# Kernel optimization log

Measured on AMD Instinct MI355X. Metric: run time of the kernel, lower is better.

Reference implementation:

```python
import jax, jax.numpy as jnp
import numpy as np

HIDDEN = 512
EMBED = 512
VOCAB = 32000
BRANCH = 4
LEVELS = 9  # level 0 = root, level LEVELS-1 = leaves (complete 4-ary tree)
N_NODES = sum(BRANCH ** l for l in range(LEVELS))  # 87381


def setup_inputs() -> dict:
    key = jax.random.key(0)
    ks = jax.random.split(key, 16)
    s = 1.0 / np.sqrt(HIDDEN)
    inp = {
        "token_ids": jax.random.randint(ks[0], (N_NODES,), 0, VOCAB, dtype=jnp.int32),
        "emb": jax.random.normal(ks[1], (VOCAB, EMBED), jnp.float32) * 0.02,
        "Wi": jax.random.normal(ks[2], (EMBED, HIDDEN), jnp.float32) * s,
        "Ui": jax.random.normal(ks[3], (HIDDEN, HIDDEN), jnp.float32) * s,
        "bi": jnp.zeros((HIDDEN,), jnp.float32),
        "Wf": jax.random.normal(ks[4], (EMBED, HIDDEN), jnp.float32) * s,
        "Uf": jax.random.normal(ks[5], (HIDDEN, HIDDEN), jnp.float32) * s,
        "bf": jnp.zeros((HIDDEN,), jnp.float32),
        "Wo": jax.random.normal(ks[6], (EMBED, HIDDEN), jnp.float32) * s,
        "Uo": jax.random.normal(ks[7], (HIDDEN, HIDDEN), jnp.float32) * s,
        "bo": jnp.zeros((HIDDEN,), jnp.float32),
        "Wu": jax.random.normal(ks[8], (EMBED, HIDDEN), jnp.float32) * s,
        "Uu": jax.random.normal(ks[9], (HIDDEN, HIDDEN), jnp.float32) * s,
        "bu": jnp.zeros((HIDDEN,), jnp.float32),
        "branching": BRANCH,
        "n_levels": LEVELS,
    }
    return inp


def reference(token_ids, emb, Wi, Ui, bi, Wf, Uf, bf, Wo, Uo, bo, Wu, Uu, bu,
              branching, n_levels):
    # Level-synchronous Child-Sum Tree-LSTM over a complete `branching`-ary tree.
    # token_ids is laid out level by level, root first.
    B = int(branching)
    L = int(n_levels)
    H = Wi.shape[1]
    level_sizes = [B ** l for l in range(L)]
    offsets = np.concatenate([[0], np.cumsum(level_sizes)])  # static Python ints

    # Leaves: original code sets h = c = 0 (leaf embedding is computed but unused).
    h = jnp.zeros((level_sizes[-1], H), dtype=emb.dtype)
    c = jnp.zeros((level_sizes[-1], H), dtype=emb.dtype)
    hs_levels = [h]  # hidden states collected leaves -> root (level order)

    for l in range(L - 2, -1, -1):
        n = level_sizes[l]
        x = jnp.take(emb, token_ids[offsets[l]:offsets[l + 1]], axis=0)  # [n, E]
        ch_h = h.reshape(n, B, H)  # children of node k are contiguous
        ch_c = c.reshape(n, B, H)
        h_tilde = ch_h.sum(axis=1)  # [n, H] child-sum
        i = jax.nn.sigmoid(x @ Wi + h_tilde @ Ui + bi)
        # per-child forget gates: [n, B, H]
        f = jax.nn.sigmoid((x @ Wf + bf)[:, None, :] + ch_h @ Uf)
        o = jax.nn.sigmoid(x @ Wo + h_tilde @ Uo + bo)
        u = jnp.tanh(x @ Wu + h_tilde @ Uu + bu)
        c = i * u + (f * ch_c).sum(axis=1)
        h = o * jnp.tanh(c)
        hs_levels.append(h)

    hidden_states = jnp.concatenate(hs_levels, axis=0)  # [N_NODES, H]
    return hidden_states, h, c  # h, c are the root states, shape [1, H]
```

## Files before the change

### kernel.cpp

```cpp
#include <hip/hip_runtime.h>

#define DI __device__ __forceinline__

typedef __attribute__((ext_vector_type(8))) __bf16 bf16x8;
typedef __attribute__((ext_vector_type(4))) float f32x4;
typedef __attribute__((ext_vector_type(8))) unsigned short ushort8;
typedef unsigned long long ull;

static DI unsigned short f2b(float f) {
  unsigned int x = __builtin_bit_cast(unsigned int, f);
  unsigned int r = (x + 0x7FFFu + ((x >> 16) & 1u)) >> 16;
  return (unsigned short)r;
}
static DI float b2f(unsigned short u) {
  return __builtin_bit_cast(float, (unsigned int)u << 16);
}
static DI float sigmf(float x) { return 1.0f / (1.0f + __expf(-x)); }

typedef const __attribute__((address_space(1))) void* gcptr;
typedef __attribute__((address_space(3))) void* lptr;
static DI void gl_lds16(const void* g, void* l) {
  __builtin_amdgcn_global_load_lds((gcptr)g, (lptr)l, 16, 0, 0);
}

#define GCOL(g, d) ((((d) >> 5) << 7) + ((g) << 5) + ((d) & 31))

static DI size_t qaddr(int NT, int row4, int c) {
  int tm = row4 >> 5, tn = c >> 7;
  int rq = row4 & 31, c7 = c & 127;
  int wv = ((rq >> 4) << 1) | (c7 >> 6);
  int mf = (rq >> 2) & 3, nf = (c7 >> 4) & 3;
  int lane = ((rq & 3) << 4) | (c7 & 15);
  return ((size_t)(tm * NT + tn) << 12) + (size_t)((((wv << 4) + (mf << 2) + nf) << 6) + lane);
}

__global__ void prep_pack(const float* __restrict__ Wi, const float* __restrict__ Ui,
                          const float* __restrict__ bi, const float* __restrict__ Wf,
                          const float* __restrict__ Uf, const float* __restrict__ bfv,
                          const float* __restrict__ Wo, const float* __restrict__ Uo,
                          const float* __restrict__ bo, const float* __restrict__ Wu,
                          const float* __restrict__ Uu, const float* __restrict__ bu,
                          unsigned short* __restrict__ Wp, unsigned short* __restrict__ Upiou,
                          unsigned short* __restrict__ Upf, float* __restrict__ bias)
{
  int u = blockIdx.x * blockDim.x + threadIdx.x;
  if (u < 131072) {
    int k8 = u >> 11, n = u & 2047;
    int gate = (n >> 5) & 3;
    int d = ((n >> 7) << 5) | (n & 31);
    const float* W = (gate == 0) ? Wi : (gate == 1) ? Wf : (gate == 2) ? Wo : Wu;
    ushort8 pk;
    #pragma unroll
    for (int t = 0; t < 8; ++t) pk[t] = f2b(W[(size_t)(k8*8+t)*512 + d]);
    *(ushort8*)&Wp[(size_t)u*8] = pk;
  } else if (u < 131072 + 98304) {
    int v = u - 131072;
    int k8 = v / 1536, n = v - k8*1536;
    const float* U = (n < 512) ? Ui : (n < 1024) ? Uo : Uu;
    int c = n & 511;
    ushort8 pk;
    #pragma unroll
    for (int t = 0; t < 8; ++t) pk[t] = f2b(U[(size_t)(k8*8+t)*512 + c]);
    *(ushort8*)&Upiou[(size_t)v*8] = pk;
  } else {
    int v = u - 229376;
    int k8 = v >> 9, c = v & 511;
    ushort8 pk;
    #pragma unroll
    for (int t = 0; t < 8; ++t) pk[t] = f2b(Uf[(size_t)(k8*8+t)*512 + c]);
    *(ushort8*)&Upf[(size_t)v*8] = pk;
  }
  if (u < 2048) {
    int gate = (u >> 5) & 3;
    int d = ((u >> 7) << 5) | (u & 31);
    bias[u] = (gate == 0) ? bi[d] : (gate == 1) ? bfv[d] : (gate == 2) ? bo[d] : bu[d];
  }
}

__global__ void gather_x(const int* __restrict__ tok, const float* __restrict__ emb,
                         unsigned short* __restrict__ X)
{
  int u = blockIdx.x * blockDim.x + threadIdx.x;
  if (u >= 22272*64) return;
  int R = u >> 6, ch = u & 63;
  int l, node;
  if (R < 512)       { l = R >> 7; node = R & 127; int sz = 1 << (2*l); if (node >= sz) node = sz - 1; }
  else if (R < 768)  { l = 4; node = R - 512; }
  else if (R < 1792) { l = 5; node = R - 768; }
  else if (R < 5888) { l = 6; node = R - 1792; }
  else               { l = 7; node = R - 5888; }
  static const int offs_c[8] = {0,1,5,21,85,341,1365,5461};
  int tk = tok[offs_c[l] + node];
  const float* src = emb + (size_t)tk*512 + ch*8;
  ushort8 pk;
  #pragma unroll
  for (int t = 0; t < 8; ++t) pk[t] = f2b(src[t]);
  *(ushort8*)&X[(size_t)u*8] = pk;
}

struct GDesc {
  const unsigned short* A;
  const unsigned short* Bp;
  ull* C;
  int M, N, NT;
};
struct L7P {
  float* hout; unsigned short* hb; float* cb; unsigned short* ht;
  float* zbase; size_t z4;
};

template<bool FUSED>
__global__ __launch_bounds__(256)
void gemm512(GDesc g1, GDesc g2, int split, const float* __restrict__ bias, L7P l7)
{
  __shared__ float smemf[128*132];
  unsigned short* As = (unsigned short*)smemf;
  unsigned short* Bs = (unsigned short*)smemf + 2*128*64;

  const int nwg = gridDim.x, orig = blockIdx.x;
  const int q = nwg >> 3, r = nwg & 7;
  const int xcd = orig & 7, idx = orig >> 3;
  const int wg = (xcd < r ? xcd*(q+1) : r*(q+1) + (xcd-r)*q) + idx;

  const bool role1 = (wg < split);
  GDesc g = role1 ? g1 : g2;
  const int lwg = role1 ? wg : wg - split;
  const int tm = lwg / g.NT, tn = lwg - tm * g.NT;

  const int tid = threadIdx.x;
  const int wave = tid >> 6, lane = tid & 63;
  const int Mbase = tm * 128, Nbase = tn * 128;
  const int wr = wave >> 1, wc = wave & 1;

  const int arow_l = wave*8 + (lane >> 3);
  const int acol8  = lane & 7;
  const int sw8    = arow_l & 7;

  f32x4 acc[4][4] = {};

  auto STAGE = [&](int p, int k0) {
    #pragma unroll
    for (int c = 0; c < 4; ++c) {
      int grow = Mbase + c*32 + arow_l;
      if (grow >= g.M) grow = g.M - 1;
      gl_lds16(g.A + (size_t)grow*512 + k0 + ((acol8 ^ sw8) * 8),
               As + p*(128*64) + (c*32 + wave*8)*64);
    }
    #pragma unroll
    for (int c = 0; c < 4; ++c) {
      int k8 = c*2 + (wave >> 1);
      int colh = (wave & 1) * 64;
      gl_lds16(g.Bp + ((size_t)((k0 >> 3) + k8) * g.N + Nbase + colh + lane) * 8,
               Bs + p*(8*128*8) + (k8*128 + colh)*8);
    }
  };

  auto COMPUTE = [&](int p) {
    #pragma unroll
    for (int ks = 0; ks < 2; ++ks) {
      bf16x8 af[4], bfr[4];
      #pragma unroll
      for (int mf = 0; mf < 4; ++mf) {
        int row = wr*64 + mf*16 + (lane & 15);
        int kc  = ks*4 + (lane >> 4);
        af[mf] = *(const bf16x8*)&As[p*(128*64) + row*64 + ((kc ^ (row & 7)) * 8)];
      }
      #pragma unroll
      for (int nf = 0; nf < 4; ++nf) {
        int col = wc*64 + nf*16 + (lane & 15);
        int k8  = ks*4 + (lane >> 4);
        bfr[nf] = *(const bf16x8*)&Bs[p*(8*128*8) + (k8*128 + col) * 8];
      }
      #pragma unroll
      for (int mf = 0; mf < 4; ++mf)
        #pragma unroll
        for (int nf = 0; nf < 4; ++nf)
          acc[mf][nf] = __builtin_amdgcn_mfma_f32_16x16x32_bf16(af[mf], bfr[nf], acc[mf][nf], 0, 0, 0);
    }
  };

  STAGE(0, 0);
  __syncthreads();
  #pragma unroll
  for (int it = 0; it < 7; ++it) {
    STAGE((it + 1) & 1, (it + 1) * 64);
    COMPUTE(it & 1);
    __syncthreads();
  }
  COMPUTE(1);

  auto ZERO_DUTY = [&]() {
    if constexpr (FUSED) {
      size_t b4 = (size_t)orig * 3072;
      f32x4 z = {0.f, 0.f, 0.f, 0.f};
      f32x4* zp = (f32x4*)l7.zbase;
      #pragma unroll
      for (int i = 0; i < 12; ++i) {
        size_t off = b4 + (size_t)i*256 + tid;
        if (off < l7.z4) zp[off] = z;
      }
    }
  };

  if (FUSED && tm >= 46) {
    __syncthreads();
    #pragma unroll
    for (int mf = 0; mf < 4; ++mf) {
      int rbase = wr*64 + mf*16 + (lane >> 4)*4;
      #pragma unroll
      for (int nf = 0; nf < 4; ++nf) {
        int col = wc*64 + nf*16 + (lane & 15);
        #pragma unroll
        for (int rr = 0; rr < 4; ++rr)
          smemf[(rbase + rr)*132 + col] = acc[mf][nf][rr];
      }
    }
    __syncthreads();
    ZERO_DUTY();
    const int dlow = tid & 31, rowg = tid >> 5;
    const int d = tn*32 + dlow;
    const float bi_ = bias[tn*128      + dlow];
    const float bo_ = bias[tn*128 + 64 + dlow];
    const float bu_ = bias[tn*128 + 96 + dlow];
    const int nodebase = Mbase - 5888 + rowg*16;
    float hts = 0.f;
    #pragma unroll
    for (int rr = 0; rr < 16; ++rr) {
      int lrow = rowg*16 + rr;
      float gi = smemf[lrow*132      + dlow];
      float go = smemf[lrow*132 + 64 + dlow];
      float gu = smemf[lrow*132 + 96 + dlow];
      float iv = sigmf(gi + bi_), ov = sigmf(go + bo_), uv = tanhf(gu + bu_);
      float cv = iv * uv;
      float hv = ov * tanhf(cv);
      size_t node = nodebase + rr;
      l7.hout[node*512 + d] = hv;
      l7.hb[node*512 + d]   = f2b(hv);
      l7.cb[node*512 + d]   = cv;
      hts += hv;
      if ((rr & 3) == 3) {
        l7.ht[(size_t)((nodebase + rr - 3) >> 2)*512 + d] = f2b(hts);
        hts = 0.f;
      }
    }
  } else {
    ZERO_DUTY();
    float bv[4];
    #pragma unroll
    for (int nf = 0; nf < 4; ++nf)
      bv[nf] = (bias != nullptr && role1) ? bias[Nbase + wc*64 + nf*16 + (lane & 15)] : 0.f;
    ull* Cb = g.C + ((size_t)(tm * g.NT + tn) << 12) + ((size_t)wave << 10);
    #pragma unroll
    for (int mf = 0; mf < 4; ++mf)
      #pragma unroll
      for (int nf = 0; nf < 4; ++nf) {
        f32x4 a = acc[mf][nf];
        ull pk = (ull)f2b(a[0] + bv[nf]) | ((ull)f2b(a[1] + bv[nf]) << 16)
               | ((ull)f2b(a[2] + bv[nf]) << 32) | ((ull)f2b(a[3] + bv[nf]) << 48);
        Cb[(mf*4 + nf)*64 + lane] = pk;
      }
  }
}

__global__ __launch_bounds__(256)
void combine2(const ull* __restrict__ Gq,
              const ull* __restrict__ Rq,
              const ull* __restrict__ Fq,
              const float* __restrict__ cch,
              float* __restrict__ hout,
              unsigned short* __restrict__ hbf,
              float* __restrict__ cout,
              unsigned short* __restrict__ htout,
              float* __restrict__ rootx,
              int n)
{
  const int b = blockIdx.x, t = threadIdx.x;
  #pragma unroll
  for (int half = 0; half < 2; ++half) {
    const int c = t + half * 256;
    ull gi4 = Gq[qaddr(16, b, GCOL(0, c))];
    ull gf4 = Gq[qaddr(16, b, GCOL(1, c))];
    ull go4 = Gq[qaddr(16, b, GCOL(2, c))];
    ull gu4 = Gq[qaddr(16, b, GCOL(3, c))];
    ull ri4 = Rq[qaddr(12, b, c)];
    ull ro4 = Rq[qaddr(12, b, c + 512)];
    ull ru4 = Rq[qaddr(12, b, c + 1024)];
    float hts = 0.f;
    #pragma unroll
    for (int rI = 0; rI < 4; ++rI) {
      int j = b*4 + rI;
      float gi = b2f((unsigned short)(gi4 >> (16*rI)));
      float gf = b2f((unsigned short)(gf4 >> (16*rI)));
      float go = b2f((unsigned short)(go4 >> (16*rI)));
      float gu = b2f((unsigned short)(gu4 >> (16*rI)));
      float iv = sigmf(gi + b2f((unsigned short)(ri4 >> (16*rI))));
      float ov = sigmf(go + b2f((unsigned short)(ro4 >> (16*rI))));
      float uv = tanhf(gu + b2f((unsigned short)(ru4 >> (16*rI))));
      ull f4 = Fq[qaddr(4, j, c)];
      const float* cc = cch + (size_t)(j*4)*512 + c;
      float fs = 0.f;
      #pragma unroll
      for (int k = 0; k < 4; ++k)
        fs += sigmf(gf + b2f((unsigned short)(f4 >> (16*k)))) * cc[(size_t)k*512];
      float cv = iv*uv + fs;
      float hv = ov * tanhf(cv);
      if (j < n) {
        hout[(size_t)j*512 + c] = hv;
        hbf[(size_t)j*512 + c]  = f2b(hv);
        cout[(size_t)j*512 + c] = cv;
        if (rootx && j == 0) { rootx[c] = hv; rootx[512 + c] = cv; }
        hts += hv;
      }
    }
    if (htout) htout[(size_t)b*512 + c] = f2b(hts);
  }
}

extern "C" void kernel_launch(void* const* d_in, const int* in_sizes, int n_in,
                              void* d_out, int out_size, void* d_ws, size_t ws_size,
                              hipStream_t stream)
{
  const int*   tok = (const int*)d_in[0];
  const float* emb = (const float*)d_in[1];
  const float* Wi  = (const float*)d_in[2];
  const float* Ui  = (const float*)d_in[3];
  const float* bi  = (const float*)d_in[4];
  const float* Wf  = (const float*)d_in[5];
  const float* Uf  = (const float*)d_in[6];
  const float* bfv = (const float*)d_in[7];
  const float* Wo  = (const float*)d_in[8];
  const float* Uo  = (const float*)d_in[9];
  const float* bo  = (const float*)d_in[10];
  const float* Wu  = (const float*)d_in[11];
  const float* Uu  = (const float*)d_in[12];
  const float* bu  = (const float*)d_in[13];

  char* ws = (char*)d_ws;
  unsigned short* Wp    = (unsigned short*)(ws + 0);
  unsigned short* Upiou = (unsigned short*)(ws + 2097152);
  unsigned short* Upf   = (unsigned short*)(ws + 3670016);
  float*          bias  = (float*)        (ws + 4194304);
  unsigned short* hbf   = (unsigned short*)(ws + 4202496);
  unsigned short* htbf  = (unsigned short*)(ws + 26571776);
  float*          cbuf  = (float*)        (ws + 32163840);
  ull*            RiouQ = (ull*)          (ws + 76902400);
  ull*            RfQ   = (ull*)          (ws + 89485312);
  ull*            Gq    = (ull*)          (ws + 106262528);
  unsigned short* X     = (unsigned short*)(ws + 130379776);

  float* fout = (float*)d_out;

  static const int  offs[9]    = {0,1,5,21,85,341,1365,5461,21845};
  static const int  padbase[8] = {0,128,256,384,512,768,1792,5888};
  static const long outoff[8]  = {87380,87376,87360,87296,87040,86016,81920,65536};

  prep_pack<<<1024, 256, 0, stream>>>(Wi,Ui,bi,Wf,Uf,bfv,Wo,Uo,bo,Wu,Uu,bu,
                                      Wp,Upiou,Upf,bias);
  gather_x<<<(22272*64)/256, 256, 0, stream>>>(tok, emb, X);

  GDesc gA { X, Wp, Gq, 22272, 2048, 16 };
  L7P l7 { fout + (size_t)outoff[7]*512, hbf + (size_t)offs[7]*512,
           cbuf + (size_t)offs[7]*512, htbf + (size_t)offs[6]*512,
           fout, (size_t)65536*512/4 };
  gemm512<true><<<174*16, 256, 0, stream>>>(gA, gA, 174*16, bias, l7);

  L7P l7n {};
  for (int l = 6; l >= 0; --l) {
    int n = 1 << (2*l);
    int tm1 = (n + 127) / 128, tm2 = (4*n + 127) / 128;
    int split = tm1 * 12;
    GDesc g1 { htbf + (size_t)offs[l]*512,   Upiou, RiouQ, n,   1536, 12 };
    GDesc g2 { hbf  + (size_t)offs[l+1]*512, Upf,   RfQ,   4*n, 512,  4  };
    gemm512<false><<<split + tm2*4, 256, 0, stream>>>(g1, g2, split, nullptr, l7n);
    combine2<<<(n + 3) / 4, 256, 0, stream>>>(
        Gq + (size_t)padbase[l]*512, RiouQ, RfQ, cbuf + (size_t)offs[l+1]*512,
        fout + (size_t)outoff[l]*512, hbf + (size_t)offs[l]*512, cbuf + (size_t)offs[l]*512,
        (l > 0) ? htbf + (size_t)offs[l-1]*512 : nullptr,
        (l == 0) ? fout + (size_t)87381*512 : nullptr,
        n);
  }
}
```

Before: 259.7 us.

## Interleave gates at 16-column granularity and fuse level-7 epilogue in registers

Changes the packed gate column layout from 32-wide to 16-wide groups, so each wave's MFMA output fragment holds all four gates for the same hidden columns. The level-7 epilogue can then compute the LSTM cell directly from accumulators, with no LDS round trip or extra barriers. The GEMM K-step is halved to 32, which shrinks the LDS footprint but doubles the number of pipeline iterations and syncs. Higher occupancy from smaller LDS is traded against more barrier overhead and less strided epilogue stores.

```diff
diff --git a/kernel.cpp b/kernel.cpp
--- a/kernel.cpp
+++ b/kernel.cpp
@@ -23,7 +23,7 @@
   __builtin_amdgcn_global_load_lds((gcptr)g, (lptr)l, 16, 0, 0);
 }
 
-#define GCOL(g, d) ((((d) >> 5) << 7) + ((g) << 5) + ((d) & 31))
+#define GCOL(g, d) ((((d) >> 4) << 6) + ((g) << 4) + ((d) & 15))
 
 static DI size_t qaddr(int NT, int row4, int c) {
   int tm = row4 >> 5, tn = c >> 7;
@@ -46,8 +46,8 @@
   int u = blockIdx.x * blockDim.x + threadIdx.x;
   if (u < 131072) {
     int k8 = u >> 11, n = u & 2047;
-    int gate = (n >> 5) & 3;
-    int d = ((n >> 7) << 5) | (n & 31);
+    int gate = (n >> 4) & 3;
+    int d = ((n >> 6) << 4) | (n & 15);
     const float* W = (gate == 0) ? Wi : (gate == 1) ? Wf : (gate == 2) ? Wo : Wu;
     ushort8 pk;
     #pragma unroll
@@ -71,8 +71,8 @@
     *(ushort8*)&Upf[(size_t)v*8] = pk;
   }
   if (u < 2048) {
-    int gate = (u >> 5) & 3;
-    int d = ((u >> 7) << 5) | (u & 31);
+    int gate = (u >> 4) & 3;
+    int d = ((u >> 6) << 4) | (u & 15);
     bias[u] = (gate == 0) ? bi[d] : (gate == 1) ? bfv[d] : (gate == 2) ? bo[d] : bu[d];
   }
 }
@@ -113,9 +113,8 @@
 __global__ __launch_bounds__(256)
 void gemm512(GDesc g1, GDesc g2, int split, const float* __restrict__ bias, L7P l7)
 {
-  __shared__ float smemf[128*132];
-  unsigned short* As = (unsigned short*)smemf;
-  unsigned short* Bs = (unsigned short*)smemf + 2*128*64;
+  __shared__ unsigned short As[2*128*32];
+  __shared__ unsigned short Bs[2*4*128*8];
 
   const int nwg = gridDim.x, orig = blockIdx.x;
   const int q = nwg >> 3, r = nwg & 7;
@@ -132,58 +131,49 @@
   const int Mbase = tm * 128, Nbase = tn * 128;
   const int wr = wave >> 1, wc = wave & 1;
 
-  const int arow_l = wave*8 + (lane >> 3);
-  const int acol8  = lane & 7;
-  const int sw8    = arow_l & 7;
-
   f32x4 acc[4][4] = {};
 
   auto STAGE = [&](int p, int k0) {
     #pragma unroll
-    for (int c = 0; c < 4; ++c) {
-      int grow = Mbase + c*32 + arow_l;
-      if (grow >= g.M) grow = g.M - 1;
-      gl_lds16(g.A + (size_t)grow*512 + k0 + ((acol8 ^ sw8) * 8),
-               As + p*(128*64) + (c*32 + wave*8)*64);
-    }
-    #pragma unroll
-    for (int c = 0; c < 4; ++c) {
-      int k8 = c*2 + (wave >> 1);
-      int colh = (wave & 1) * 64;
-      gl_lds16(g.Bp + ((size_t)((k0 >> 3) + k8) * g.N + Nbase + colh + lane) * 8,
-               Bs + p*(8*128*8) + (k8*128 + colh)*8);
+    for (int c = 0; c < 2; ++c) {
+      int lrow = c*64 + wave*16 + (lane >> 2);
+      int grow = Mbase + lrow; if (grow >= g.M) grow = g.M - 1;
+      gl_lds16(g.A + (size_t)grow*512 + k0 + (((lane & 3) ^ (lrow & 3)) * 8),
+               As + p*(128*32) + (c*64 + wave*16)*32);
+    }
+    #pragma unroll
+    for (int c = 0; c < 2; ++c) {
+      gl_lds16(g.Bp + ((size_t)((k0 >> 3) + wave) * g.N + Nbase + c*64 + lane) * 8,
+               Bs + p*(4*128*8) + (wave*128 + c*64)*8);
     }
   };
 
   auto COMPUTE = [&](int p) {
-    #pragma unroll
-    for (int ks = 0; ks < 2; ++ks) {
-      bf16x8 af[4], bfr[4];
-      #pragma unroll
-      for (int mf = 0; mf < 4; ++mf) {
-        int row = wr*64 + mf*16 + (lane & 15);
-        int kc  = ks*4 + (lane >> 4);
-        af[mf] = *(const bf16x8*)&As[p*(128*64) + row*64 + ((kc ^ (row & 7)) * 8)];
-      }
-      #pragma unroll
-      for (int nf = 0; nf < 4; ++nf) {
-        int col = wc*64 + nf*16 + (lane & 15);
-        int k8  = ks*4 + (lane >> 4);
-        bfr[nf] = *(const bf16x8*)&Bs[p*(8*128*8) + (k8*128 + col) * 8];
-      }
-      #pragma unroll
-      for (int mf = 0; mf < 4; ++mf)
-        #pragma unroll
-        for (int nf = 0; nf < 4; ++nf)
-          acc[mf][nf] = __builtin_amdgcn_mfma_f32_16x16x32_bf16(af[mf], bfr[nf], acc[mf][nf], 0, 0, 0);
-    }
+    bf16x8 af[4], bfr[4];
+    #pragma unroll
+    for (int mf = 0; mf < 4; ++mf) {
+      int row = wr*64 + mf*16 + (lane & 15);
+      int kc  = lane >> 4;
+      af[mf] = *(const bf16x8*)&As[p*(128*32) + row*32 + ((kc ^ (row & 3)) * 8)];
+    }
+    #pragma unroll
+    for (int nf = 0; nf < 4; ++nf) {
+      int col = wc*64 + nf*16 + (lane & 15);
+      int k8  = lane >> 4;
+      bfr[nf] = *(const bf16x8*)&Bs[p*(4*128*8) + (k8*128 + col) * 8];
+    }
+    #pragma unroll
+    for (int mf = 0; mf < 4; ++mf)
+      #pragma unroll
+      for (int nf = 0; nf < 4; ++nf)
+        acc[mf][nf] = __builtin_amdgcn_mfma_f32_16x16x32_bf16(af[mf], bfr[nf], acc[mf][nf], 0, 0, 0);
   };
 
   STAGE(0, 0);
   __syncthreads();
   #pragma unroll
-  for (int it = 0; it < 7; ++it) {
-    STAGE((it + 1) & 1, (it + 1) * 64);
+  for (int it = 0; it < 15; ++it) {
+    STAGE((it + 1) & 1, (it + 1) * 32);
     COMPUTE(it & 1);
     __syncthreads();
   }
@@ -203,46 +193,31 @@
   };
 
   if (FUSED && tm >= 46) {
-    __syncthreads();
+    const int dlow = lane & 15;
+    const float bi_ = bias[Nbase + wc*64      + dlow];
+    const float bo_ = bias[Nbase + wc*64 + 32 + dlow];
+    const float bu_ = bias[Nbase + wc*64 + 48 + dlow];
+    const int d = tn*32 + wc*16 + dlow;
     #pragma unroll
     for (int mf = 0; mf < 4; ++mf) {
-      int rbase = wr*64 + mf*16 + (lane >> 4)*4;
-      #pragma unroll
-      for (int nf = 0; nf < 4; ++nf) {
-        int col = wc*64 + nf*16 + (lane & 15);
-        #pragma unroll
-        for (int rr = 0; rr < 4; ++rr)
-          smemf[(rbase + rr)*132 + col] = acc[mf][nf][rr];
+      int node0 = Mbase - 5888 + wr*64 + mf*16 + (lane >> 4)*4;
+      float hts = 0.f;
+      #pragma unroll
+      for (int rr = 0; rr < 4; ++rr) {
+        float iv = sigmf(acc[mf][0][rr] + bi_);
+        float ov = sigmf(acc[mf][2][rr] + bo_);
+        float uv = tanhf(acc[mf][3][rr] + bu_);
+        float cv = iv * uv;
+        float hv = ov * tanhf(cv);
+        size_t node = node0 + rr;
+        l7.hout[node*512 + d] = hv;
+        l7.hb[node*512 + d]   = f2b(hv);
+        l7.cb[node*512 + d]   = cv;
+        hts += hv;
       }
-    }
-    __syncthreads();
+      l7.ht[(size_t)(node0 >> 2)*512 + d] = f2b(hts);
+    }
     ZERO_DUTY();
-    const int dlow = tid & 31, rowg = tid >> 5;
-    const int d = tn*32 + dlow;
-    const float bi_ = bias[tn*128      + dlow];
-    const float bo_ = bias[tn*128 + 64 + dlow];
-    const float bu_ = bias[tn*128 + 96 + dlow];
-    const int nodebase = Mbase - 5888 + rowg*16;
-    float hts = 0.f;
-    #pragma unroll
-    for (int rr = 0; rr < 16; ++rr) {
-      int lrow = rowg*16 + rr;
-      float gi = smemf[lrow*132      + dlow];
-      float go = smemf[lrow*132 + 64 + dlow];
-      float gu = smemf[lrow*132 + 96 + dlow];
-      float iv = sigmf(gi + bi_), ov = sigmf(go + bo_), uv = tanhf(gu + bu_);
-      float cv = iv * uv;
-      float hv = ov * tanhf(cv);
-      size_t node = nodebase + rr;
-      l7.hout[node*512 + d] = hv;
-      l7.hb[node*512 + d]   = f2b(hv);
-      l7.cb[node*512 + d]   = cv;
-      hts += hv;
-      if ((rr & 3) == 3) {
-        l7.ht[(size_t)((nodebase + rr - 3) >> 2)*512 + d] = f2b(hts);
-        hts = 0.f;
-      }
-    }
   } else {
     ZERO_DUTY();
     float bv[4];
```

New measurement: 307.1 us. +18.2%, slower.

## Fuse small upper tree levels into one persistent kernel with grid barriers

Applied to the files above, without the earlier changes.

Replaces the per-level GEMM and combine launches for levels 4..0 with a single 64-block persistent kernel. It uses atomic grid barriers and a direct-from-global tile GEMM, which removes many small kernel launches and their gaps. The fused leaf-level epilogue now works on accumulator registers, using a reordered gate interleave instead of an LDS round-trip. Output zeroing moves into the level-6 GEMM. The spin barriers rely on all 64 blocks being co-resident.

```diff
diff --git a/kernel.cpp b/kernel.cpp
--- a/kernel.cpp
+++ b/kernel.cpp
@@ -23,7 +23,7 @@
   __builtin_amdgcn_global_load_lds((gcptr)g, (lptr)l, 16, 0, 0);
 }
 
-#define GCOL(g, d) ((((d) >> 5) << 7) + ((g) << 5) + ((d) & 31))
+#define GCOL(g, d) ((((d) >> 4) << 6) + ((g) << 4) + ((d) & 15))
 
 static DI size_t qaddr(int NT, int row4, int c) {
   int tm = row4 >> 5, tn = c >> 7;
@@ -41,13 +41,15 @@
                           const float* __restrict__ bo, const float* __restrict__ Wu,
                           const float* __restrict__ Uu, const float* __restrict__ bu,
                           unsigned short* __restrict__ Wp, unsigned short* __restrict__ Upiou,
-                          unsigned short* __restrict__ Upf, float* __restrict__ bias)
+                          unsigned short* __restrict__ Upf, float* __restrict__ bias,
+                          unsigned int* __restrict__ bar)
 {
   int u = blockIdx.x * blockDim.x + threadIdx.x;
+  if (u < 16) bar[u] = 0u;
   if (u < 131072) {
     int k8 = u >> 11, n = u & 2047;
-    int gate = (n >> 5) & 3;
-    int d = ((n >> 7) << 5) | (n & 31);
+    int gate = (n >> 4) & 3;
+    int d = ((n >> 6) << 4) | (n & 15);
     const float* W = (gate == 0) ? Wi : (gate == 1) ? Wf : (gate == 2) ? Wo : Wu;
     ushort8 pk;
     #pragma unroll
@@ -71,8 +73,8 @@
     *(ushort8*)&Upf[(size_t)v*8] = pk;
   }
   if (u < 2048) {
-    int gate = (u >> 5) & 3;
-    int d = ((u >> 7) << 5) | (u & 31);
+    int gate = (u >> 4) & 3;
+    int d = ((u >> 6) << 4) | (u & 15);
     bias[u] = (gate == 0) ? bi[d] : (gate == 1) ? bfv[d] : (gate == 2) ? bo[d] : bu[d];
   }
 }
@@ -106,16 +108,15 @@
 };
 struct L7P {
   float* hout; unsigned short* hb; float* cb; unsigned short* ht;
-  float* zbase; size_t z4;
 };
 
 template<bool FUSED>
 __global__ __launch_bounds__(256)
-void gemm512(GDesc g1, GDesc g2, int split, const float* __restrict__ bias, L7P l7)
-{
-  __shared__ float smemf[128*132];
-  unsigned short* As = (unsigned short*)smemf;
-  unsigned short* Bs = (unsigned short*)smemf + 2*128*64;
+void gemm512(GDesc g1, GDesc g2, int split, const float* __restrict__ bias, L7P l7,
+             float* __restrict__ zbase, size_t z4)
+{
+  __shared__ unsigned short As[2*128*64];
+  __shared__ unsigned short Bs[2*8*128*8];
 
   const int nwg = gridDim.x, orig = blockIdx.x;
   const int q = nwg >> 3, r = nwg & 7;
@@ -131,6 +132,7 @@
   const int wave = tid >> 6, lane = tid & 63;
   const int Mbase = tm * 128, Nbase = tn * 128;
   const int wr = wave >> 1, wc = wave & 1;
+  const int l15 = lane & 15, l4 = lane >> 4;
 
   const int arow_l = wave*8 + (lane >> 3);
   const int acol8  = lane & 7;
@@ -161,14 +163,14 @@
       bf16x8 af[4], bfr[4];
       #pragma unroll
       for (int mf = 0; mf < 4; ++mf) {
-        int row = wr*64 + mf*16 + (lane & 15);
-        int kc  = ks*4 + (lane >> 4);
+        int row = wr*64 + mf*16 + l15;
+        int kc  = ks*4 + l4;
         af[mf] = *(const bf16x8*)&As[p*(128*64) + row*64 + ((kc ^ (row & 7)) * 8)];
       }
       #pragma unroll
       for (int nf = 0; nf < 4; ++nf) {
-        int col = wc*64 + nf*16 + (lane & 15);
-        int k8  = ks*4 + (lane >> 4);
+        int col = wc*64 + nf*16 + l15;
+        int k8  = ks*4 + l4;
         bfr[nf] = *(const bf16x8*)&Bs[p*(8*128*8) + (k8*128 + col) * 8];
       }
       #pragma unroll
@@ -189,66 +191,35 @@
   }
   COMPUTE(1);
 
-  auto ZERO_DUTY = [&]() {
-    if constexpr (FUSED) {
-      size_t b4 = (size_t)orig * 3072;
-      f32x4 z = {0.f, 0.f, 0.f, 0.f};
-      f32x4* zp = (f32x4*)l7.zbase;
-      #pragma unroll
-      for (int i = 0; i < 12; ++i) {
-        size_t off = b4 + (size_t)i*256 + tid;
-        if (off < l7.z4) zp[off] = z;
+  if (FUSED && tm >= 46) {
+    const float bi_ = bias[Nbase + wc*64      + l15];
+    const float bo_ = bias[Nbase + wc*64 + 32 + l15];
+    const float bu_ = bias[Nbase + wc*64 + 48 + l15];
+    const int d = tn*32 + wc*16 + l15;
+    #pragma unroll
+    for (int mf = 0; mf < 4; ++mf) {
+      int node0 = Mbase - 5888 + wr*64 + mf*16 + l4*4;
+      float hts = 0.f;
+      #pragma unroll
+      for (int rr = 0; rr < 4; ++rr) {
+        float iv = sigmf(acc[mf][0][rr] + bi_);
+        float ov = sigmf(acc[mf][2][rr] + bo_);
+        float uv = tanhf(acc[mf][3][rr] + bu_);
+        float cv = iv * uv;
+        float hv = ov * tanhf(cv);
+        size_t node = node0 + rr;
+        l7.hout[node*512 + d] = hv;
+        l7.hb[node*512 + d]   = f2b(hv);
+        l7.cb[node*512 + d]   = cv;
+        hts += hv;
       }
-    }
-  };
-
-  if (FUSED && tm >= 46) {
-    __syncthreads();
-    #pragma unroll
-    for (int mf = 0; mf < 4; ++mf) {
-      int rbase = wr*64 + mf*16 + (lane >> 4)*4;
-      #pragma unroll
-      for (int nf = 0; nf < 4; ++nf) {
-        int col = wc*64 + nf*16 + (lane & 15);
-        #pragma unroll
-        for (int rr = 0; rr < 4; ++rr)
-          smemf[(rbase + rr)*132 + col] = acc[mf][nf][rr];
-      }
-    }
-    __syncthreads();
-    ZERO_DUTY();
-    const int dlow = tid & 31, rowg = tid >> 5;
-    const int d = tn*32 + dlow;
-    const float bi_ = bias[tn*128      + dlow];
-    const float bo_ = bias[tn*128 + 64 + dlow];
-    const float bu_ = bias[tn*128 + 96 + dlow];
-    const int nodebase = Mbase - 5888 + rowg*16;
-    float hts = 0.f;
-    #pragma unroll
-    for (int rr = 0; rr < 16; ++rr) {
-      int lrow = rowg*16 + rr;
-      float gi = smemf[lrow*132      + dlow];
-      float go = smemf[lrow*132 + 64 + dlow];
-      float gu = smemf[lrow*132 + 96 + dlow];
-      float iv = sigmf(gi + bi_), ov = sigmf(go + bo_), uv = tanhf(gu + bu_);
-      float cv = iv * uv;
-      float hv = ov * tanhf(cv);
-      size_t node = nodebase + rr;
-      l7.hout[node*512 + d] = hv;
-      l7.hb[node*512 + d]   = f2b(hv);
-      l7.cb[node*512 + d]   = cv;
-      hts += hv;
-      if ((rr & 3) == 3) {
-        l7.ht[(size_t)((nodebase + rr - 3) >> 2)*512 + d] = f2b(hts);
-        hts = 0.f;
-      }
+      l7.ht[(size_t)(node0 >> 2)*512 + d] = f2b(hts);
     }
   } else {
-    ZERO_DUTY();
     float bv[4];
     #pragma unroll
     for (int nf = 0; nf < 4; ++nf)
-      bv[nf] = (bias != nullptr && role1) ? bias[Nbase + wc*64 + nf*16 + (lane & 15)] : 0.f;
+      bv[nf] = (bias != nullptr && role1) ? bias[Nbase + wc*64 + nf*16 + l15] : 0.f;
     ull* Cb = g.C + ((size_t)(tm * g.NT + tn) << 12) + ((size_t)wave << 10);
     #pragma unroll
     for (int mf = 0; mf < 4; ++mf)
@@ -260,21 +231,21 @@
         Cb[(mf*4 + nf)*64 + lane] = pk;
       }
   }
-}
-
-__global__ __launch_bounds__(256)
-void combine2(const ull* __restrict__ Gq,
-              const ull* __restrict__ Rq,
-              const ull* __restrict__ Fq,
-              const float* __restrict__ cch,
-              float* __restrict__ hout,
-              unsigned short* __restrict__ hbf,
-              float* __restrict__ cout,
-              unsigned short* __restrict__ htout,
-              float* __restrict__ rootx,
-              int n)
-{
-  const int b = blockIdx.x, t = threadIdx.x;
+
+  if (zbase != nullptr) {
+    f32x4 z = {0.f, 0.f, 0.f, 0.f};
+    f32x4* zp = (f32x4*)zbase;
+    size_t stride = (size_t)nwg * 256;
+    for (size_t off = (size_t)orig*256 + tid; off < z4; off += stride) zp[off] = z;
+  }
+}
+
+static DI void combine_body(const ull* __restrict__ Gq, const ull* __restrict__ Rq,
+                            const ull* __restrict__ Fq, const float* __restrict__ cch,
+                            float* __restrict__ hout, unsigned short* __restrict__ hbf,
+                            float* __restrict__ cout, unsigned short* __restrict__ htout,
+                            float* __restrict__ rootx, int n, int b, int t)
+{
   #pragma unroll
   for (int half = 0; half < 2; ++half) {
     const int c = t + half * 256;
@@ -313,6 +284,108 @@
       }
     }
     if (htout) htout[(size_t)b*512 + c] = f2b(hts);
+  }
+}
+
+__global__ __launch_bounds__(256)
+void combine2(const ull* Gq, const ull* Rq, const ull* Fq, const float* cch,
+              float* hout, unsigned short* hbf, float* cout,
+              unsigned short* htout, float* rootx, int n)
+{
+  combine_body(Gq, Rq, Fq, cch, hout, hbf, cout, htout, rootx, n, blockIdx.x, threadIdx.x);
+}
+
+static DI void gbar(unsigned int* c, unsigned int target) {
+  __syncthreads();
+  if (threadIdx.x == 0) {
+    __hip_atomic_fetch_add(c, 1u, __ATOMIC_ACQ_REL, __HIP_MEMORY_SCOPE_AGENT);
+    while (__hip_atomic_load(c, __ATOMIC_ACQUIRE, __HIP_MEMORY_SCOPE_AGENT) < target) {}
+  }
+  __syncthreads();
+}
+
+static DI void tile_gemm(const unsigned short* __restrict__ A, int M,
+                         const unsigned short* __restrict__ Bp, int N, int NT,
+                         int tm, int tn, ull* __restrict__ C, int wave, int lane)
+{
+  const int wr = wave >> 1, wc = wave & 1;
+  const int l15 = lane & 15, l4 = lane >> 4;
+  size_t a0[4]; unsigned int b0[4];
+  #pragma unroll
+  for (int mf = 0; mf < 4; ++mf) {
+    int row = tm*128 + wr*64 + mf*16 + l15;
+    if (row >= M) row = M - 1;
+    a0[mf] = (size_t)row*512 + l4*8;
+  }
+  #pragma unroll
+  for (int nf = 0; nf < 4; ++nf)
+    b0[nf] = (unsigned int)(((unsigned)l4 * N + tn*128 + wc*64 + nf*16 + l15) * 8);
+  const unsigned int bstep = (unsigned int)N * 32;
+
+  f32x4 acc[4][4] = {};
+  #pragma unroll
+  for (int ks = 0; ks < 16; ++ks) {
+    bf16x8 af[4], bfr[4];
+    #pragma unroll
+    for (int mf = 0; mf < 4; ++mf) af[mf] = *(const bf16x8*)(A + a0[mf] + ks*32);
+    #pragma unroll
+    for (int nf = 0; nf < 4; ++nf) bfr[nf] = *(const bf16x8*)(Bp + b0[nf] + ks*bstep);
+    #pragma unroll
+    for (int mf = 0; mf < 4; ++mf)
+      #pragma unroll
+      for (int nf = 0; nf < 4; ++nf)
+        acc[mf][nf] = __builtin_amdgcn_mfma_f32_16x16x32_bf16(af[mf], bfr[nf], acc[mf][nf], 0, 0, 0);
+  }
+  ull* Cb = C + ((size_t)(tm * NT + tn) << 12) + ((size_t)wave << 10);
+  #pragma unroll
+  for (int mf = 0; mf < 4; ++mf)
+    #pragma unroll
+    for (int nf = 0; nf < 4; ++nf) {
+      f32x4 a = acc[mf][nf];
+      ull pk = (ull)f2b(a[0]) | ((ull)f2b(a[1]) << 16)
+             | ((ull)f2b(a[2]) << 32) | ((ull)f2b(a[3]) << 48);
+      Cb[(mf*4 + nf)*64 + lane] = pk;
+    }
+}
+
+__global__ __launch_bounds__(256)
+void mega(const unsigned short* __restrict__ hbf, const unsigned short* __restrict__ htbf,
+          float* __restrict__ cbuf, const unsigned short* __restrict__ Upiou,
+          const unsigned short* __restrict__ Upf, ull* __restrict__ RiouQ,
+          ull* __restrict__ RfQ, const ull* __restrict__ Gq, float* __restrict__ fout,
+          unsigned int* __restrict__ bar)
+{
+  static const int offs_c[9]   = {0,1,5,21,85,341,1365,5461,21845};
+  static const int padbase_c[8]= {0,128,256,384,512,768,1792,5888};
+  static const int outoff_c[8] = {87380,87376,87360,87296,87040,86016,81920,65536};
+  const int b = blockIdx.x, t = threadIdx.x;
+  const unsigned int NB = gridDim.x;
+  int phase = 0;
+  for (int l = 4; l >= 0; --l) {
+    const int n = 1 << (2*l);
+    const int t1 = ((n + 127) >> 7) * 12;
+    const int t2 = ((4*n + 127) >> 7) * 4;
+    const int wave = t >> 6, lane = t & 63;
+    if (b < t1) {
+      tile_gemm(htbf + (size_t)offs_c[l]*512, n, Upiou, 1536, 12, b/12, b%12,
+                RiouQ, wave, lane);
+    } else if (b < t1 + t2) {
+      int bb = b - t1;
+      tile_gemm(hbf + (size_t)offs_c[l+1]*512, 4*n, Upf, 512, 4, bb/4, bb%4,
+                RfQ, wave, lane);
+    }
+    gbar(bar + phase, NB); ++phase;
+    if (b < (n + 3) / 4) {
+      combine_body(Gq + (size_t)padbase_c[l]*512, RiouQ, RfQ,
+                   cbuf + (size_t)offs_c[l+1]*512,
+                   fout + (size_t)outoff_c[l]*512,
+                   (unsigned short*)(hbf + (size_t)offs_c[l]*512),
+                   cbuf + (size_t)offs_c[l]*512,
+                   (l > 0) ? (unsigned short*)(htbf + (size_t)offs_c[l-1]*512) : nullptr,
+                   (l == 0) ? fout + (size_t)87381*512 : nullptr,
+                   n, b, t);
+    }
+    if (l > 0) { gbar(bar + phase, NB); ++phase; }
   }
 }
 
@@ -340,13 +413,14 @@
   unsigned short* Upiou = (unsigned short*)(ws + 2097152);
   unsigned short* Upf   = (unsigned short*)(ws + 3670016);
   float*          bias  = (float*)        (ws + 4194304);
-  unsigned short* hbf   = (unsigned short*)(ws + 4202496);
-  unsigned short* htbf  = (unsigned short*)(ws + 26571776);
-  float*          cbuf  = (float*)        (ws + 32163840);
-  ull*            RiouQ = (ull*)          (ws + 76902400);
-  ull*            RfQ   = (ull*)          (ws + 89485312);
-  ull*            Gq    = (ull*)          (ws + 106262528);
-  unsigned short* X     = (unsigned short*)(ws + 130379776);
+  unsigned int*   bar   = (unsigned int*) (ws + 4202496);
+  unsigned short* hbf   = (unsigned short*)(ws + 4202752);
+  unsigned short* htbf  = (unsigned short*)(ws + 26572032);
+  float*          cbuf  = (float*)        (ws + 32164096);
+  ull*            RiouQ = (ull*)          (ws + 76902656);
+  ull*            RfQ   = (ull*)          (ws + 89485568);
+  ull*            Gq    = (ull*)          (ws + 106262784);
+  unsigned short* X     = (unsigned short*)(ws + 130380032);
 
   float* fout = (float*)d_out;
 
@@ -355,28 +429,33 @@
   static const long outoff[8]  = {87380,87376,87360,87296,87040,86016,81920,65536};
 
   prep_pack<<<1024, 256, 0, stream>>>(Wi,Ui,bi,Wf,Uf,bfv,Wo,Uo,bo,Wu,Uu,bu,
-                                      Wp,Upiou,Upf,bias);
+                                      Wp,Upiou,Upf,bias,bar);
   gather_x<<<(22272*64)/256, 256, 0, stream>>>(tok, emb, X);
 
   GDesc gA { X, Wp, Gq, 22272, 2048, 16 };
   L7P l7 { fout + (size_t)outoff[7]*512, hbf + (size_t)offs[7]*512,
-           cbuf + (size_t)offs[7]*512, htbf + (size_t)offs[6]*512,
-           fout, (size_t)65536*512/4 };
-  gemm512<true><<<174*16, 256, 0, stream>>>(gA, gA, 174*16, bias, l7);
+           cbuf + (size_t)offs[7]*512, htbf + (size_t)offs[6]*512 };
+  gemm512<true><<<174*16, 256, 0, stream>>>(gA, gA, 174*16, bias, l7, nullptr, 0);
 
   L7P l7n {};
-  for (int l = 6; l >= 0; --l) {
-    int n = 1 << (2*l);
-    int tm1 = (n + 127) / 128, tm2 = (4*n + 127) / 128;
-    int split = tm1 * 12;
-    GDesc g1 { htbf + (size_t)offs[l]*512,   Upiou, RiouQ, n,   1536, 12 };
-    GDesc g2 { hbf  + (size_t)offs[l+1]*512, Upf,   RfQ,   4*n, 512,  4  };
-    gemm512<false><<<split + tm2*4, 256, 0, stream>>>(g1, g2, split, nullptr, l7n);
-    combine2<<<(n + 3) / 4, 256, 0, stream>>>(
-        Gq + (size_t)padbase[l]*512, RiouQ, RfQ, cbuf + (size_t)offs[l+1]*512,
-        fout + (size_t)outoff[l]*512, hbf + (size_t)offs[l]*512, cbuf + (size_t)offs[l]*512,
-        (l > 0) ? htbf + (size_t)offs[l-1]*512 : nullptr,
-        (l == 0) ? fout + (size_t)87381*512 : nullptr,
-        n);
-  }
-}
+  {
+    GDesc g1 { htbf + (size_t)offs[6]*512, Upiou, RiouQ, 4096,  1536, 12 };
+    GDesc g2 { hbf  + (size_t)offs[7]*512, Upf,   RfQ,   16384, 512,  4  };
+    gemm512<false><<<32*12 + 128*4, 256, 0, stream>>>(g1, g2, 32*12, nullptr, l7n,
+                                                      fout, (size_t)65536*512/4);
+    combine2<<<1024, 256, 0, stream>>>(
+        Gq + (size_t)padbase[6]*512, RiouQ, RfQ, cbuf + (size_t)offs[7]*512,
+        fout + (size_t)outoff[6]*512, hbf + (size_t)offs[6]*512, cbuf + (size_t)offs[6]*512,
+        htbf + (size_t)offs[5]*512, nullptr, 4096);
+  }
+  {
+    GDesc g1 { htbf + (size_t)offs[5]*512, Upiou, RiouQ, 1024, 1536, 12 };
+    GDesc g2 { hbf  + (size_t)offs[6]*512, Upf,   RfQ,   4096, 512,  4  };
+    gemm512<false><<<8*12 + 32*4, 256, 0, stream>>>(g1, g2, 8*12, nullptr, l7n, nullptr, 0);
+    combine2<<<256, 256, 0, stream>>>(
+        Gq + (size_t)padbase[5]*512, RiouQ, RfQ, cbuf + (size_t)offs[6]*512,
+        fout + (size_t)outoff[5]*512, hbf + (size_t)offs[5]*512, cbuf + (size_t)offs[5]*512,
+        htbf + (size_t)offs[4]*512, nullptr, 1024);
+  }
+  mega<<<64, 256, 0, stream>>>(hbf, htbf, cbuf, Upiou, Upf, RiouQ, RfQ, Gq, fout, bar);
+}
```

Result: slower. 361.8 us (+39.3%).
